# Kernel tuning notes

Hardware: AMD Instinct MI355X
Metric: run time of the kernel (lower is better)

The kernel has to match this reference:

```python
import jax, jax.numpy as jnp
import numpy as np

TAU = 0.1  # args.aggregator_tau
EPS = 1e-12  # F.normalize default eps


def _l2_normalize(x):
    n = jnp.linalg.norm(x, axis=1, keepdims=True)
    return x / jnp.maximum(n, EPS)


def setup_inputs() -> dict:
    key = jax.random.key(0)
    ks = jax.random.split(key, 7)
    d, C = 128, 100
    n_lb, n_ulb = 2048, 7168
    return {
        "anchor_feat": jax.random.normal(ks[0], (n_ulb, d), dtype=jnp.float32),
        "positive_feat": jax.random.normal(ks[1], (n_ulb, d), dtype=jnp.float32),
        "lb_feat": jax.random.normal(ks[2], (n_lb, d), dtype=jnp.float32),
        "lb_one_hot": jax.random.uniform(ks[3], (n_lb, C), dtype=jnp.float32),
        "logits_x_lb": jax.random.normal(ks[4], (n_lb, C), dtype=jnp.float32),
        "logits_x_ulb_1": jax.random.normal(ks[5], (n_ulb, C), dtype=jnp.float32),
        "logits_x_ulb_2": jax.random.normal(ks[6], (n_ulb, C), dtype=jnp.float32),
    }


def reference(anchor_feat, positive_feat, lb_feat, lb_one_hot,
              logits_x_lb, logits_x_ulb_1, logits_x_ulb_2):
    # flags baked in: softmax_class_label=True, one_hot_class_label=True, T=1.0
    # [N, d] shared query/key matrix, N = n_lb + 2*n_ulb
    feats = _l2_normalize(jnp.concatenate([lb_feat, anchor_feat, positive_feat], axis=0))
    logits_x_ulb = jnp.concatenate([logits_x_ulb_1, logits_x_ulb_2], axis=0)
    prob_xulb = jax.nn.softmax(logits_x_ulb, axis=-1)
    class_val = jnp.concatenate([lb_one_hot, prob_xulb], axis=0)  # [N, C]
    # soft-kNN attention: softmax over NxN cosine sims, then weighted avg of probs
    attn = jax.nn.softmax(jnp.einsum('id,jd->ij', feats, feats) / TAU, axis=1)
    logits_x_lb_ulb = attn @ class_val  # [N, C]
    n_lb = logits_x_lb.shape[0]
    out_lb = logits_x_lb_ulb[:n_lb]
    ulb = logits_x_lb_ulb[n_lb:]
    n_ulb = ulb.shape[0] // 2
    return (anchor_feat, positive_feat, lb_feat, lb_one_hot,
            out_lb, ulb[:n_ulb], ulb[n_ulb:])
```

## Files before the change

### kernel.cpp

```cpp
#include <hip/hip_runtime.h>
#include <hip/hip_bf16.h>
#include <stdint.h>

#define N_TOT   16384
#define N_LB    2048
#define C_DIM   100

typedef __attribute__((ext_vector_type(8))) short s16x8;
typedef __attribute__((ext_vector_type(4))) float f32x4;

#if __has_builtin(__builtin_amdgcn_exp2f)
#define EXP2F __builtin_amdgcn_exp2f
#else
#define EXP2F exp2f
#endif

__device__ __forceinline__ short f2bf(float x) {
  union { float f; unsigned u; } v; v.f = x;
  unsigned r = (v.u + 0x7fffu + ((v.u >> 16) & 1u)) >> 16;
  return (short)r;
}
__device__ __forceinline__ float bf2f(short h) {
  union { unsigned u; float f; } v; v.u = ((unsigned)(unsigned short)h) << 16; return v.f;
}
__device__ __forceinline__ int slotsw(int c, int q) {
  return (c ^ q ^ ((q & 8) >> 1)) & 15;
}
__device__ __forceinline__ unsigned cvtpk_bf16(float a, float b) {
  unsigned r;
  asm("v_cvt_pk_bf16_f32 %0, %1, %2" : "=v"(r) : "v"(a), "v"(b));
  return r;
}

__global__ __launch_bounds__(256) void k_prep(const float* __restrict__ anc,
                                              const float* __restrict__ pos,
                                              const float* __restrict__ lbf,
                                              const float* __restrict__ onehot,
                                              const float* __restrict__ lg1,
                                              const float* __restrict__ lg2,
                                              short* __restrict__ feats_ws,
                                              short* __restrict__ v_ws,
                                              float* __restrict__ out) {
  const int bid = blockIdx.x, tid = threadIdx.x;
  const int wid = tid >> 6, lane = tid & 63;
  if (bid < 4096) {
    const int r = bid * 4 + wid;
    const float* src = (r < N_LB) ? (lbf + (size_t)r * 128)
                     : ((r < 9216) ? (anc + (size_t)(r - 2048) * 128)
                                   : (pos + (size_t)(r - 9216) * 128));
    float2 x = *(const float2*)(src + lane * 2);
    float ss = x.x * x.x + x.y * x.y;
    #pragma unroll
    for (int o = 32; o; o >>= 1) ss += __shfl_xor(ss, o);
    float scale = rsqrtf(fmaxf(ss, 1e-24f));
    const int kt = r >> 4, q = r & 15;
    union { short s[2]; unsigned u; } w;
    w.s[0] = f2bf(x.x * scale);
    w.s[1] = f2bf(x.y * scale);
    *(unsigned*)(feats_ws + (size_t)kt * 2048 + q * 128 +
                 (slotsw(lane >> 2, q) << 3) + ((lane & 3) << 1)) = w.u;
  } else if (bid < 8192) {
    const int r = (bid - 4096) * 4 + wid;
    const int c0 = lane, c1 = lane + 64;
    float v0, v1;
    if (r < N_LB) {
      v0 = (c0 < C_DIM) ? onehot[(size_t)r * C_DIM + c0] : 0.f;
      v1 = (c1 < C_DIM) ? onehot[(size_t)r * C_DIM + c1] : 0.f;
    } else {
      const float* lr = (r < 9216) ? (lg1 + (size_t)(r - 2048) * C_DIM)
                                   : (lg2 + (size_t)(r - 9216) * C_DIM);
      float x0 = (c0 < C_DIM) ? lr[c0] : -3e38f;
      float x1 = (c1 < C_DIM) ? lr[c1] : -3e38f;
      float m = fmaxf(x0, x1);
      #pragma unroll
      for (int o = 32; o; o >>= 1) m = fmaxf(m, __shfl_xor(m, o));
      float e0 = (c0 < C_DIM) ? EXP2F((x0 - m) * 1.44269504f) : 0.f;
      float e1 = (c1 < C_DIM) ? EXP2F((x1 - m) * 1.44269504f) : 0.f;
      float s = e0 + e1;
      #pragma unroll
      for (int o = 32; o; o >>= 1) s += __shfl_xor(s, o);
      float inv = 1.0f / s;
      v0 = e0 * inv;
      v1 = e1 * inv;
    }
    if (c1 == 112) v1 = 1.0f;
    const int T = r >> 5, rr = r & 31;
    const int jj = (((rr >> 4) & 1) << 2) | (rr & 3);
    const int gg = (rr & 15) >> 2;
    {
      const int ch = c0 >> 4, qq = c0 & 15;
      v_ws[(size_t)T * 4096 + ch * 512 + gg * 128 + ((qq ^ (gg << 2)) << 3) + jj] = f2bf(v0);
    }
    {
      const int ch = c1 >> 4, qq = c1 & 15;
      v_ws[(size_t)T * 4096 + ch * 512 + gg * 128 + ((qq ^ (gg << 2)) << 3) + jj] = f2bf(v1);
    }
  } else {
    const long long i4 = (long long)(bid - 8192) * 256 + tid;
    const long long f = i4 * 4;
    float4 v;
    if (f < 917504)        v = *(const float4*)(anc + f);
    else if (f < 1835008)  v = *(const float4*)(pos + (f - 917504));
    else if (f < 2097152)  v = *(const float4*)(lbf + (f - 1835008));
    else                   v = *(const float4*)(onehot + (f - 2097152));
    *(float4*)(out + f) = v;
  }
}

__device__ __forceinline__ void stage64(const short* kg, short* dst, int wave, int lane) {
  #pragma unroll
  for (int i = 0; i < 4; ++i) {
    const int blk = wave * 4 + i;
    __builtin_amdgcn_global_load_lds(
        (const __attribute__((address_space(1))) void*)(kg + blk * 512 + lane * 8),
        (__attribute__((address_space(3))) void*)(dst + blk * 512), 16, 0, 0);
  }
}

__global__ __launch_bounds__(256, 2) void k_attn(const short* __restrict__ feats,
                                                 const short* __restrict__ vws,
                                                 short* __restrict__ pO,
                                                 float* __restrict__ pL,
                                                 float* __restrict__ outp,
                                                 int S, int nt2) {
  __shared__ __align__(16) short lk[2][8192];
  const int tid = threadIdx.x;
  const int wave = tid >> 6, lane = tid & 63;
  const int q = lane & 15, g = lane >> 4;
  const int bid = blockIdx.x;
  const int slice = bid % S;
  const int qsup = (bid / S) * 4 + wave;
  const int t0h = slice * nt2;

  s16x8 bQ[2][4];
  #pragma unroll
  for (int set = 0; set < 2; ++set)
    #pragma unroll
    for (int kk = 0; kk < 4; ++kk)
      bQ[set][kk] = *(const s16x8*)(feats + (size_t)(qsup * 2 + set) * 2048 + q * 128 +
                                    (slotsw((kk << 2) | g, q) << 3));

  f32x4 zero = {0.f, 0.f, 0.f, 0.f};
  f32x4 oacc[2][8];
  #pragma unroll
  for (int set = 0; set < 2; ++set)
    #pragma unroll
    for (int c = 0; c < 8; ++c) oacc[set][c] = zero;

  int dso[4];
  #pragma unroll
  for (int kk = 0; kk < 4; ++kk) dso[kk] = q * 128 + (slotsw((kk << 2) | g, q) << 3);
  const int vfo = g * 128 + ((q ^ (g << 2)) << 3);

  stage64(feats + (size_t)t0h * 8192, lk[0], wave, lane);
  __syncthreads();

  for (int t = 0; t < nt2; ++t) {
    const int cur = t & 1;
    if (t + 1 < nt2)
      stage64(feats + (size_t)(t0h + t + 1) * 8192, lk[cur ^ 1], wave, lane);
    const short* lkc = lk[cur];
    const short* vb = vws + (size_t)(t0h + t) * 8192 + vfo;

    s16x8 aK0[4], aK1[4];
    #pragma unroll
    for (int kk = 0; kk < 4; ++kk) {
      aK0[kk] = *(const s16x8*)(lkc + dso[kk]);
      aK1[kk] = *(const s16x8*)(lkc + 2048 + dso[kk]);
    }
    f32x4 sA0[2] = {zero, zero}, sA1[2] = {zero, zero};
    __builtin_amdgcn_s_setprio(1);
    #pragma unroll
    for (int kk = 0; kk < 4; ++kk)
      #pragma unroll
      for (int set = 0; set < 2; ++set) {
        sA0[set] = __builtin_amdgcn_mfma_f32_16x16x32_bf16(aK0[kk], bQ[set][kk], sA0[set], 0, 0, 0);
        sA1[set] = __builtin_amdgcn_mfma_f32_16x16x32_bf16(aK1[kk], bQ[set][kk], sA1[set], 0, 0, 0);
      }
    __builtin_amdgcn_s_setprio(0);

    s16x8 bV0[8];
    #pragma unroll
    for (int c = 0; c < 8; ++c) bV0[c] = *(const s16x8*)(vb + c * 512);

    s16x8 bK0[4], bK1[4];
    #pragma unroll
    for (int kk = 0; kk < 4; ++kk) {
      bK0[kk] = *(const s16x8*)(lkc + 4096 + dso[kk]);
      bK1[kk] = *(const s16x8*)(lkc + 6144 + dso[kk]);
    }
    f32x4 sB0[2] = {zero, zero}, sB1[2] = {zero, zero};
    __builtin_amdgcn_s_setprio(1);
    #pragma unroll
    for (int kk = 0; kk < 4; ++kk)
      #pragma unroll
      for (int set = 0; set < 2; ++set) {
        sB0[set] = __builtin_amdgcn_mfma_f32_16x16x32_bf16(bK0[kk], bQ[set][kk], sB0[set], 0, 0, 0);
        sB1[set] = __builtin_amdgcn_mfma_f32_16x16x32_bf16(bK1[kk], bQ[set][kk], sB1[set], 0, 0, 0);
      }
    __builtin_amdgcn_s_setprio(0);

    s16x8 pf0[2];
    #pragma unroll
    for (int set = 0; set < 2; ++set) {
      union { unsigned w[4]; s16x8 h; } pu;
      #pragma unroll
      for (int rp = 0; rp < 2; ++rp) {
        float pa = EXP2F(sA0[set][2 * rp]     * 14.4269504f - 14.4269504f);
        float pb = EXP2F(sA0[set][2 * rp + 1] * 14.4269504f - 14.4269504f);
        float pc = EXP2F(sA1[set][2 * rp]     * 14.4269504f - 14.4269504f);
        float pd = EXP2F(sA1[set][2 * rp + 1] * 14.4269504f - 14.4269504f);
        pu.w[rp]     = cvtpk_bf16(pa, pb);
        pu.w[rp + 2] = cvtpk_bf16(pc, pd);
      }
      pf0[set] = pu.h;
    }

    s16x8 bV1[8];
    #pragma unroll
    for (int c = 0; c < 8; ++c) bV1[c] = *(const s16x8*)(vb + 4096 + c * 512);

    __builtin_amdgcn_s_setprio(1);
    #pragma unroll
    for (int c = 0; c < 8; ++c)
      #pragma unroll
      for (int set = 0; set < 2; ++set)
        oacc[set][c] = __builtin_amdgcn_mfma_f32_16x16x32_bf16(pf0[set], bV0[c], oacc[set][c], 0, 0, 0);
    __builtin_amdgcn_s_setprio(0);

    s16x8 pf1[2];
    #pragma unroll
    for (int set = 0; set < 2; ++set) {
      union { unsigned w[4]; s16x8 h; } pu;
      #pragma unroll
      for (int rp = 0; rp < 2; ++rp) {
        float pa = EXP2F(sB0[set][2 * rp]     * 14.4269504f - 14.4269504f);
        float pb = EXP2F(sB0[set][2 * rp + 1] * 14.4269504f - 14.4269504f);
        float pc = EXP2F(sB1[set][2 * rp]     * 14.4269504f - 14.4269504f);
        float pd = EXP2F(sB1[set][2 * rp + 1] * 14.4269504f - 14.4269504f);
        pu.w[rp]     = cvtpk_bf16(pa, pb);
        pu.w[rp + 2] = cvtpk_bf16(pc, pd);
      }
      pf1[set] = pu.h;
    }

    __builtin_amdgcn_s_setprio(1);
    #pragma unroll
    for (int c = 0; c < 8; ++c)
      #pragma unroll
      for (int set = 0; set < 2; ++set)
        oacc[set][c] = __builtin_amdgcn_mfma_f32_16x16x32_bf16(pf1[set], bV1[c], oacc[set][c], 0, 0, 0);
    __builtin_amdgcn_s_setprio(0);

    __syncthreads();
  }

  #pragma unroll
  for (int set = 0; set < 2; ++set) {
    const int row0 = qsup * 32 + set * 16;
    if (S == 1) {
      float linv[4];
      #pragma unroll
      for (int r = 0; r < 4; ++r) linv[r] = 1.0f / __shfl(oacc[set][7][r], g << 4);
      #pragma unroll
      for (int c = 0; c < 7; ++c) {
        const int col = c * 16 + q;
        if (col < C_DIM)
          #pragma unroll
          for (int r = 0; r < 4; ++r)
            outp[(size_t)(row0 + (g << 2) + r) * C_DIM + col] = oacc[set][c][r] * linv[r];
      }
    } else {
      if (q == 0)
        #pragma unroll
        for (int r = 0; r < 4; ++r)
          pL[(size_t)slice * N_TOT + row0 + (g << 2) + r] = oacc[set][7][r];
      #pragma unroll
      for (int c = 0; c < 7; ++c)
        #pragma unroll
        for (int r = 0; r < 4; ++r)
          pO[((size_t)slice * N_TOT + row0 + (g << 2) + r) * 112 + c * 16 + q] =
              f2bf(oacc[set][c][r]);
    }
  }
}

__global__ void k_combine(const short* __restrict__ pO, const float* __restrict__ pL,
                          float* __restrict__ out, int S) {
  const int row = blockIdx.x * 2 + (threadIdx.x >> 7);
  const int c = threadIdx.x & 127;
  float l = 0.f, o = 0.f;
  for (int s = 0; s < S; ++s) {
    l += pL[(size_t)s * N_TOT + row];
    if (c < 112) o += bf2f(pO[((size_t)s * N_TOT + row) * 112 + c]);
  }
  if (c < C_DIM) out[(size_t)row * C_DIM + c] = o / l;
}

extern "C" void kernel_launch(void* const* d_in, const int* in_sizes, int n_in,
                              void* d_out, int out_size, void* d_ws, size_t ws_size,
                              hipStream_t stream) {
  const float* anchor   = (const float*)d_in[0];
  const float* positive = (const float*)d_in[1];
  const float* lb_feat  = (const float*)d_in[2];
  const float* lb_onehot= (const float*)d_in[3];
  const float* lg1      = (const float*)d_in[5];
  const float* lg2      = (const float*)d_in[6];
  float* out = (float*)d_out;

  short* feats_ws = (short*)d_ws;
  short* v_ws     = feats_ws + 2097152;
  float* pL       = (float*)(v_ws + 2097152);
  short* pO       = (short*)(pL + 8 * N_TOT);

  int S = 8;
  while (S > 1 && 8912896ull + (size_t)S * N_TOT * 112 * 2 > ws_size) S >>= 1;
  const int nt2 = (512 / S) >> 1;

  k_prep<<<10440, 256, 0, stream>>>(anchor, positive, lb_feat, lb_onehot, lg1, lg2,
                                    feats_ws, v_ws, out);

  float* attn_out = out + 2301952;
  k_attn<<<128 * S, 256, 0, stream>>>(feats_ws, v_ws, pO, pL, attn_out, S, nt2);
  if (S > 1)
    k_combine<<<N_TOT / 2, 256, 0, stream>>>(pO, pL, attn_out, S);
}
```

Before: 149.7 us.

## Compute softmax row sums in registers instead of an extra ones-column MFMA

The attention kernel no longer writes a ones column into V to get the softmax denominator through the PV MFMA. It sums the exponentiated probabilities in fp32 registers and reduces them with lane shuffles at the end. This drops one of eight output column tiles, cutting PV MFMAs and V loads by an eighth and freeing accumulator registers. The loop is also folded into two identical sub-steps, and the launch bound is raised to target three blocks per CU. The risk is register spills under the tighter bound, plus a changed shuffle layout for the row sums that must match the MFMA output rows.

New measurement: 178.2 us. 19.0% more time.

```diff
diff --git a/kernel.cpp b/kernel.cpp
--- a/kernel.cpp
+++ b/kernel.cpp
@@ -83,7 +83,6 @@
       v0 = e0 * inv;
       v1 = e1 * inv;
     }
-    if (c1 == 112) v1 = 1.0f;
     const int T = r >> 5, rr = r & 31;
     const int jj = (((rr >> 4) & 1) << 2) | (rr & 3);
     const int gg = (rr & 15) >> 2;
@@ -117,7 +116,7 @@
   }
 }
 
-__global__ __launch_bounds__(256, 2) void k_attn(const short* __restrict__ feats,
+__global__ __launch_bounds__(256, 3) void k_attn(const short* __restrict__ feats,
                                                  const short* __restrict__ vws,
                                                  short* __restrict__ pO,
                                                  float* __restrict__ pL,
@@ -141,11 +140,12 @@
                                     (slotsw((kk << 2) | g, q) << 3));
 
   f32x4 zero = {0.f, 0.f, 0.f, 0.f};
-  f32x4 oacc[2][8];
+  f32x4 oacc[2][7];
   #pragma unroll
   for (int set = 0; set < 2; ++set)
     #pragma unroll
-    for (int c = 0; c < 8; ++c) oacc[set][c] = zero;
+    for (int c = 0; c < 7; ++c) oacc[set][c] = zero;
+  float lsum[2] = {0.f, 0.f};
 
   int dso[4];
   #pragma unroll
@@ -162,106 +162,69 @@
     const short* lkc = lk[cur];
     const short* vb = vws + (size_t)(t0h + t) * 8192 + vfo;
 
-    s16x8 aK0[4], aK1[4];
-    #pragma unroll
-    for (int kk = 0; kk < 4; ++kk) {
-      aK0[kk] = *(const s16x8*)(lkc + dso[kk]);
-      aK1[kk] = *(const s16x8*)(lkc + 2048 + dso[kk]);
-    }
-    f32x4 sA0[2] = {zero, zero}, sA1[2] = {zero, zero};
-    __builtin_amdgcn_s_setprio(1);
-    #pragma unroll
-    for (int kk = 0; kk < 4; ++kk)
+    #pragma unroll
+    for (int sub = 0; sub < 2; ++sub) {
+      const short* lks = lkc + sub * 4096;
+      s16x8 aK0[4], aK1[4];
+      #pragma unroll
+      for (int kk = 0; kk < 4; ++kk) {
+        aK0[kk] = *(const s16x8*)(lks + dso[kk]);
+        aK1[kk] = *(const s16x8*)(lks + 2048 + dso[kk]);
+      }
+      s16x8 bV[7];
+      #pragma unroll
+      for (int c = 0; c < 7; ++c) bV[c] = *(const s16x8*)(vb + sub * 4096 + c * 512);
+
+      f32x4 s0[2] = {zero, zero}, s1[2] = {zero, zero};
+      __builtin_amdgcn_s_setprio(1);
+      #pragma unroll
+      for (int kk = 0; kk < 4; ++kk)
+        #pragma unroll
+        for (int set = 0; set < 2; ++set) {
+          s0[set] = __builtin_amdgcn_mfma_f32_16x16x32_bf16(aK0[kk], bQ[set][kk], s0[set], 0, 0, 0);
+          s1[set] = __builtin_amdgcn_mfma_f32_16x16x32_bf16(aK1[kk], bQ[set][kk], s1[set], 0, 0, 0);
+        }
+      __builtin_amdgcn_s_setprio(0);
+
+      s16x8 pf[2];
       #pragma unroll
       for (int set = 0; set < 2; ++set) {
-        sA0[set] = __builtin_amdgcn_mfma_f32_16x16x32_bf16(aK0[kk], bQ[set][kk], sA0[set], 0, 0, 0);
-        sA1[set] = __builtin_amdgcn_mfma_f32_16x16x32_bf16(aK1[kk], bQ[set][kk], sA1[set], 0, 0, 0);
+        float p[8];
+        #pragma unroll
+        for (int r = 0; r < 4; ++r) {
+          p[r]     = EXP2F(s0[set][r] * 14.4269504f - 14.4269504f);
+          p[r + 4] = EXP2F(s1[set][r] * 14.4269504f - 14.4269504f);
+        }
+        lsum[set] += ((p[0] + p[1]) + (p[2] + p[3])) + ((p[4] + p[5]) + (p[6] + p[7]));
+        union { unsigned w[4]; s16x8 h; } pu;
+        pu.w[0] = cvtpk_bf16(p[0], p[1]);
+        pu.w[1] = cvtpk_bf16(p[2], p[3]);
+        pu.w[2] = cvtpk_bf16(p[4], p[5]);
+        pu.w[3] = cvtpk_bf16(p[6], p[7]);
+        pf[set] = pu.h;
       }
-    __builtin_amdgcn_s_setprio(0);
-
-    s16x8 bV0[8];
-    #pragma unroll
-    for (int c = 0; c < 8; ++c) bV0[c] = *(const s16x8*)(vb + c * 512);
-
-    s16x8 bK0[4], bK1[4];
-    #pragma unroll
-    for (int kk = 0; kk < 4; ++kk) {
-      bK0[kk] = *(const s16x8*)(lkc + 4096 + dso[kk]);
-      bK1[kk] = *(const s16x8*)(lkc + 6144 + dso[kk]);
-    }
-    f32x4 sB0[2] = {zero, zero}, sB1[2] = {zero, zero};
-    __builtin_amdgcn_s_setprio(1);
-    #pragma unroll
-    for (int kk = 0; kk < 4; ++kk)
-      #pragma unroll
-      for (int set = 0; set < 2; ++set) {
-        sB0[set] = __builtin_amdgcn_mfma_f32_16x16x32_bf16(bK0[kk], bQ[set][kk], sB0[set], 0, 0, 0);
-        sB1[set] = __builtin_amdgcn_mfma_f32_16x16x32_bf16(bK1[kk], bQ[set][kk], sB1[set], 0, 0, 0);
-      }
-    __builtin_amdgcn_s_setprio(0);
-
-    s16x8 pf0[2];
-    #pragma unroll
-    for (int set = 0; set < 2; ++set) {
-      union { unsigned w[4]; s16x8 h; } pu;
-      #pragma unroll
-      for (int rp = 0; rp < 2; ++rp) {
-        float pa = EXP2F(sA0[set][2 * rp]     * 14.4269504f - 14.4269504f);
-        float pb = EXP2F(sA0[set][2 * rp + 1] * 14.4269504f - 14.4269504f);
-        float pc = EXP2F(sA1[set][2 * rp]     * 14.4269504f - 14.4269504f);
-        float pd = EXP2F(sA1[set][2 * rp + 1] * 14.4269504f - 14.4269504f);
-        pu.w[rp]     = cvtpk_bf16(pa, pb);
-        pu.w[rp + 2] = cvtpk_bf16(pc, pd);
-      }
-      pf0[set] = pu.h;
-    }
-
-    s16x8 bV1[8];
-    #pragma unroll
-    for (int c = 0; c < 8; ++c) bV1[c] = *(const s16x8*)(vb + 4096 + c * 512);
-
-    __builtin_amdgcn_s_setprio(1);
-    #pragma unroll
-    for (int c = 0; c < 8; ++c)
-      #pragma unroll
-      for (int set = 0; set < 2; ++set)
-        oacc[set][c] = __builtin_amdgcn_mfma_f32_16x16x32_bf16(pf0[set], bV0[c], oacc[set][c], 0, 0, 0);
-    __builtin_amdgcn_s_setprio(0);
-
-    s16x8 pf1[2];
-    #pragma unroll
-    for (int set = 0; set < 2; ++set) {
-      union { unsigned w[4]; s16x8 h; } pu;
-      #pragma unroll
-      for (int rp = 0; rp < 2; ++rp) {
-        float pa = EXP2F(sB0[set][2 * rp]     * 14.4269504f - 14.4269504f);
-        float pb = EXP2F(sB0[set][2 * rp + 1] * 14.4269504f - 14.4269504f);
-        float pc = EXP2F(sB1[set][2 * rp]     * 14.4269504f - 14.4269504f);
-        float pd = EXP2F(sB1[set][2 * rp + 1] * 14.4269504f - 14.4269504f);
-        pu.w[rp]     = cvtpk_bf16(pa, pb);
-        pu.w[rp + 2] = cvtpk_bf16(pc, pd);
-      }
-      pf1[set] = pu.h;
-    }
-
-    __builtin_amdgcn_s_setprio(1);
-    #pragma unroll
-    for (int c = 0; c < 8; ++c)
-      #pragma unroll
-      for (int set = 0; set < 2; ++set)
-        oacc[set][c] = __builtin_amdgcn_mfma_f32_16x16x32_bf16(pf1[set], bV1[c], oacc[set][c], 0, 0, 0);
-    __builtin_amdgcn_s_setprio(0);
-
+
+      __builtin_amdgcn_s_setprio(1);
+      #pragma unroll
+      for (int c = 0; c < 7; ++c)
+        #pragma unroll
+        for (int set = 0; set < 2; ++set)
+          oacc[set][c] = __builtin_amdgcn_mfma_f32_16x16x32_bf16(pf[set], bV[c], oacc[set][c], 0, 0, 0);
+      __builtin_amdgcn_s_setprio(0);
+    }
     __syncthreads();
   }
 
   #pragma unroll
   for (int set = 0; set < 2; ++set) {
+    float ls = lsum[set];
+    ls += __shfl_xor(ls, 16);
+    ls += __shfl_xor(ls, 32);
     const int row0 = qsup * 32 + set * 16;
     if (S == 1) {
       float linv[4];
       #pragma unroll
-      for (int r = 0; r < 4; ++r) linv[r] = 1.0f / __shfl(oacc[set][7][r], g << 4);
+      for (int r = 0; r < 4; ++r) linv[r] = 1.0f / __shfl(ls, (g << 2) | r);
       #pragma unroll
       for (int c = 0; c < 7; ++c) {
         const int col = c * 16 + q;
@@ -271,10 +234,7 @@
             outp[(size_t)(row0 + (g << 2) + r) * C_DIM + col] = oacc[set][c][r] * linv[r];
       }
     } else {
-      if (q == 0)
-        #pragma unroll
-        for (int r = 0; r < 4; ++r)
-          pL[(size_t)slice * N_TOT + row0 + (g << 2) + r] = oacc[set][7][r];
+      if (lane < 16) pL[(size_t)slice * N_TOT + row0 + lane] = ls;
       #pragma unroll
       for (int c = 0; c < 7; ++c)
         #pragma unroll
```
